# Kernel tuning notes

Hardware: AMD Instinct MI355X
Metric: run time of the kernel (lower is better)

Reference implementation:

```python
import jax, jax.numpy as jnp
import numpy as np

GROUP_SIZE = 64
M, K, N, RANK = 4096, 4096, 4096, 32


def setup_inputs() -> dict:
    key = jax.random.key(0)
    ks = jax.random.split(key, 7)
    x = jax.random.normal(ks[0], (M, K), dtype=jnp.float32)
    # int4 weight residual in [-8, 7]
    q_w = jax.random.randint(ks[1], (K, N), -8, 8, dtype=jnp.int32)
    # positive per-group weight scales, shape (K // group_size, N)
    wscales = jax.random.uniform(ks[2], (K // GROUP_SIZE, N), dtype=jnp.float32) * 0.01 + 1e-4
    lora_down = jax.random.normal(ks[3], (K, RANK), dtype=jnp.float32) * 0.02
    lora_up = jax.random.normal(ks[4], (RANK, N), dtype=jnp.float32) * 0.02
    # smoothing factors, strictly positive
    smooth = jax.random.uniform(ks[5], (K,), dtype=jnp.float32) + 0.5
    bias = jax.random.normal(ks[6], (N,), dtype=jnp.float32)
    return {"x": x, "q_w": q_w, "wscales": wscales, "lora_down": lora_down,
            "lora_up": lora_up, "smooth": smooth, "bias": bias}


def reference(x, q_w, wscales, lora_down, lora_up, smooth, bias):
    G = GROUP_SIZE
    m, k = x.shape
    n = q_w.shape[1]
    ng = k // G  # groups along K

    # smooth activation: move outliers into weights
    x_smooth = x / smooth[None, :]

    # per-group symmetric int4 quantize + dequantize of activations
    xg = x_smooth.reshape(m, ng, G)
    ascales = jnp.maximum(jnp.max(jnp.abs(xg), axis=-1) / 7.0, 1e-8)  # (m, ng)
    qx = jnp.clip(jnp.round(xg / ascales[..., None]), -8.0, 7.0)
    x_dq = (qx * ascales[..., None]).reshape(m, k)

    # dequantize int4 weight residual: grouped along K
    W_dq = (q_w.astype(jnp.float32).reshape(ng, G, n) * wscales[:, None, :]).reshape(k, n)

    # simulated int4 GEMM + fp LoRA residual + bias
    y_main = x_dq @ W_dq
    y_lora = (x @ lora_down) @ lora_up
    return y_main + y_lora + bias[None, :]
```

## Files before the change

### kernel.cpp

```cpp
#include <hip/hip_runtime.h>
#include <hip/hip_bf16.h>
#include <stdint.h>

#define GSIZE 64
#define MDIM 4096
#define KDIM 4096
#define NDIM 4096
#define RANK 32
#define KE   4160
#define NG   64
#define NSPLIT 8

typedef __bf16 bf16x4 __attribute__((ext_vector_type(4)));
typedef __bf16 bf16x8 __attribute__((ext_vector_type(8)));
typedef float  f32x4  __attribute__((ext_vector_type(4)));

#define GPTR(p) ((__attribute__((address_space(1))) void*)(uintptr_t)(p))
#define LPTR(p) ((__attribute__((address_space(3))) void*)(p))


__global__ __launch_bounds__(256) void k_lorat(const float* __restrict__ x,
                                               const float* __restrict__ ld,
                                               float* __restrict__ tws) {
    __shared__ __attribute__((aligned(16))) char smem[10240];
    __bf16* AsL = (__bf16*)smem;
    __bf16* BsL = (__bf16*)(smem + 8192);
    int b   = blockIdx.x;
    int tid = threadIdx.x;
    int m0    = (b & 31) * 128;
    int sp    = b >> 5;
    int kbase = sp * 512;
    int lane = tid & 63;
    int wave = tid >> 6;
    int quad = lane >> 4;
    int mrow = lane & 15;

    f32x4 z = {0.f, 0.f, 0.f, 0.f};
    f32x4 acc[2][2];
    acc[0][0] = z; acc[0][1] = z; acc[1][0] = z; acc[1][1] = z;

    for (int step = 0; step < 16; ++step) {
        int kk = kbase + step * 32;
        #pragma unroll
        for (int it = 0; it < 2; ++it) {
            int slot = it * 256 + tid;
            int r = slot >> 2;
            int g = (slot & 3) ^ (r & 3);
            const float* src = x + (size_t)(m0 + r) * KDIM + kk + g * 8;
            float4 a0 = *(const float4*)src;
            float4 a1 = *(const float4*)(src + 4);
            bf16x8 v = {(__bf16)a0.x, (__bf16)a0.y, (__bf16)a0.z, (__bf16)a0.w,
                        (__bf16)a1.x, (__bf16)a1.y, (__bf16)a1.z, (__bf16)a1.w};
            *(bf16x8*)(AsL + slot * 8) = v;
        }
        #pragma unroll
        for (int i2 = 0; i2 < 4; ++i2) {
            int j = i2 * 256 + tid;
            int r = j >> 5, n = j & 31;
            BsL[n * 32 + r] = (__bf16)ld[(size_t)(kk + r) * RANK + n];
        }
        __syncthreads();
        bf16x8 av[2], bv[2];
        #pragma unroll
        for (int i = 0; i < 2; ++i) {
            int row  = wave * 32 + i * 16 + mrow;
            int slot = row * 4 + (quad ^ (row & 3));
            av[i] = *(const bf16x8*)(AsL + slot * 8);
        }
        #pragma unroll
        for (int j = 0; j < 2; ++j)
            bv[j] = *(const bf16x8*)(BsL + (j * 16 + mrow) * 32 + quad * 8);
        #pragma unroll
        for (int i = 0; i < 2; ++i)
            #pragma unroll
            for (int j = 0; j < 2; ++j)
                acc[i][j] = __builtin_amdgcn_mfma_f32_16x16x32_bf16(av[i], bv[j], acc[i][j], 0, 0, 0);
        __syncthreads();
    }
    float* tout = tws + (size_t)sp * MDIM * RANK;
    #pragma unroll
    for (int i = 0; i < 2; ++i)
        #pragma unroll
        for (int j = 0; j < 2; ++j)
            #pragma unroll
            for (int r = 0; r < 4; ++r) {
                int rowg = m0 + wave * 32 + i * 16 + quad * 4 + r;
                int col  = j * 16 + mrow;
                tout[(size_t)rowg * RANK + col] = acc[i][j][r];
            }
}

__global__ __launch_bounds__(256) void k_wprep(const int*   __restrict__ qw,
                                               const float* __restrict__ wsc,
                                               const float* __restrict__ lu,
                                               __bf16* __restrict__ Wt) {
    __shared__ __attribute__((aligned(16))) __bf16 tile[64][68];
    int widx = blockIdx.x;
    int tid  = threadIdx.x;
    int n0 = (widx & 63) * 64;
    int kt = widx >> 6;
    int k0 = kt * 64;
    int tr = tid >> 4;
    int tc = (tid & 15) * 4;
    if (kt < NG) {
        float4 ws = *(const float4*)(wsc + (size_t)kt * NDIM + n0 + tc);
        #pragma unroll
        for (int r = tr; r < 64; r += 16) {
            int4 q = *(const int4*)(qw + (size_t)(k0 + r) * NDIM + n0 + tc);
            tile[r][tc + 0] = (__bf16)((float)q.x * ws.x);
            tile[r][tc + 1] = (__bf16)((float)q.y * ws.y);
            tile[r][tc + 2] = (__bf16)((float)q.z * ws.z);
            tile[r][tc + 3] = (__bf16)((float)q.w * ws.w);
        }
    } else {
        #pragma unroll
        for (int r = tr; r < 64; r += 16) {
            if (r < RANK) {
                float4 lv = *(const float4*)(lu + (size_t)r * NDIM + n0 + tc);
                tile[r][tc + 0] = (__bf16)lv.x;
                tile[r][tc + 1] = (__bf16)lv.y;
                tile[r][tc + 2] = (__bf16)lv.z;
                tile[r][tc + 3] = (__bf16)lv.w;
            } else {
                tile[r][tc + 0] = (__bf16)0.f;
                tile[r][tc + 1] = (__bf16)0.f;
                tile[r][tc + 2] = (__bf16)0.f;
                tile[r][tc + 3] = (__bf16)0.f;
            }
        }
    }
    __syncthreads();
    int nn = tid >> 3;
    int ks = (tid & 7) * 8;
    #pragma unroll
    for (int p = 0; p < 2; ++p) {
        int n = nn + p * 32;
        bf16x8 v;
        #pragma unroll
        for (int e = 0; e < 8; ++e) v[e] = tile[ks + e][n];
        *(bf16x8*)(Wt + (size_t)(n0 + n) * KE + k0 + ks) = v;
    }
}

__global__ __launch_bounds__(256) void k_quant(const float* __restrict__ x,
                                               const float* __restrict__ smooth,
                                               __bf16* __restrict__ A) {
    int row = blockIdx.x;
    int tid = threadIdx.x;
    const float4* xr4 = (const float4*)(x + (size_t)row * KDIM);
    const float4* sm4 = (const float4*)smooth;
    __bf16* ar = A + (size_t)row * KE;
    #pragma unroll
    for (int p = 0; p < 4; ++p) {
        int i4 = p * 256 + tid;
        float4 xv = xr4[i4];
        float4 sv = sm4[i4];
        float4 xs = {xv.x * __builtin_amdgcn_rcpf(sv.x),
                     xv.y * __builtin_amdgcn_rcpf(sv.y),
                     xv.z * __builtin_amdgcn_rcpf(sv.z),
                     xv.w * __builtin_amdgcn_rcpf(sv.w)};
        float a = fmaxf(fmaxf(fabsf(xs.x), fabsf(xs.y)),
                        fmaxf(fabsf(xs.z), fabsf(xs.w)));
        #pragma unroll
        for (int off = 1; off < 16; off <<= 1)
            a = fmaxf(a, __shfl_xor(a, off, 64));
        float ascale = fmaxf(a * (1.0f / 7.0f), 1e-8f);
        float rin = __builtin_amdgcn_rcpf(ascale);
        float q0 = fminf(fmaxf(rintf(xs.x * rin), -8.f), 7.f);
        float q1 = fminf(fmaxf(rintf(xs.y * rin), -8.f), 7.f);
        float q2 = fminf(fmaxf(rintf(xs.z * rin), -8.f), 7.f);
        float q3 = fminf(fmaxf(rintf(xs.w * rin), -8.f), 7.f);
        bf16x4 av = {(__bf16)(q0 * ascale), (__bf16)(q1 * ascale),
                     (__bf16)(q2 * ascale), (__bf16)(q3 * ascale)};
        *(bf16x4*)(ar + i4 * 4) = av;
    }
}

__global__ __launch_bounds__(256) void k_fin(const float* __restrict__ tws,
                                             __bf16* __restrict__ A) {
    int idx = blockIdx.x * 256 + threadIdx.x;
    int m = idx >> 4, cq = idx & 15;
    int c = cq * 4;
    bf16x4 v = {(__bf16)0.f, (__bf16)0.f, (__bf16)0.f, (__bf16)0.f};
    if (c < RANK) {
        f32x4 s = {0.f, 0.f, 0.f, 0.f};
        #pragma unroll
        for (int sp = 0; sp < NSPLIT; ++sp) {
            f32x4 p = *(const f32x4*)(tws + ((size_t)sp * MDIM + m) * RANK + c);
            s.x += p.x; s.y += p.y; s.z += p.z; s.w += p.w;
        }
        v[0] = (__bf16)s.x; v[1] = (__bf16)s.y; v[2] = (__bf16)s.z; v[3] = (__bf16)s.w;
    }
    *(bf16x4*)(A + (size_t)m * KE + KDIM + c) = v;
}

#define NT (KE / 64)
#define HS 8192
#define BS 16384

#define STAGE(ldsbase, gb, kt, half) do {                                     \
    int _k0 = (kt) * 64;                                                      \
    _Pragma("unroll")                                                         \
    for (int _it = 0; _it < 2; ++_it) {                                       \
        int _c = _it * 512 + tid;                                             \
        int _r = _c >> 3;                                                     \
        int _g = (_c & 7) ^ (_r & 7);                                         \
        __builtin_amdgcn_global_load_lds(                                     \
            GPTR((gb) + (size_t)((half) * 128 + _r) * KE + _k0 + _g * 8),     \
            LPTR((char*)(ldsbase) + (_it * 512 + wave * 64) * 16),            \
            16, 0, 0);                                                        \
    } } while (0)

#define RD_A(dst, base, qm) do {                                              \
    _Pragma("unroll")                                                         \
    for (int _i = 0; _i < 4; ++_i) {                                          \
        int _row = (qm) * 128 + wm * 64 + _i * 16 + mrow;                     \
        dst[0][_i] = *(const bf16x8*)((const char*)(base) + _row * 128 + ga0 * 16); \
        dst[1][_i] = *(const bf16x8*)((const char*)(base) + _row * 128 + ga1 * 16); \
    } } while (0)

#define RD_B(dst, base, qn) do {                                              \
    _Pragma("unroll")                                                         \
    for (int _j = 0; _j < 2; ++_j) {                                          \
        int _row = (qn) * 128 + wn * 32 + _j * 16 + mrow;                     \
        dst[0][_j] = *(const bf16x8*)((const char*)(base) + _row * 128 + ga0 * 16); \
        dst[1][_j] = *(const bf16x8*)((const char*)(base) + _row * 128 + ga1 * 16); \
    } } while (0)

#define MMA(qm, qn, AV, BV) do {                                              \
    _Pragma("unroll")                                                         \
    for (int _i = 0; _i < 4; ++_i)                                            \
        _Pragma("unroll")                                                     \
        for (int _j = 0; _j < 2; ++_j) {                                      \
            acc[qm][qn][_i][_j] = __builtin_amdgcn_mfma_f32_16x16x32_bf16(    \
                AV[0][_i], BV[0][_j], acc[qm][qn][_i][_j], 0, 0, 0);          \
            acc[qm][qn][_i][_j] = __builtin_amdgcn_mfma_f32_16x16x32_bf16(    \
                AV[1][_i], BV[1][_j], acc[qm][qn][_i][_j], 0, 0, 0);          \
        } } while (0)

#define SBAR0() __builtin_amdgcn_sched_barrier(0)

__global__ __launch_bounds__(512, 2) void k_gemm(const __bf16* __restrict__ A,
                                                 const __bf16* __restrict__ Wt,
                                                 const float*  __restrict__ bias,
                                                 float* __restrict__ out) {
    __shared__ __attribute__((aligned(16))) __bf16 As[2 * BS];
    __shared__ __attribute__((aligned(16))) __bf16 Bs[2 * BS];
    int tid  = threadIdx.x;
    int lane = tid & 63;
    int wave = tid >> 6;
    int quad = lane >> 4;
    int mrow = lane & 15;
    int wm = wave >> 2;
    int wn = wave & 3;

    int lin = blockIdx.y * 16 + blockIdx.x;
    int swz = (lin & 7) * 32 + (lin >> 3);
    int m0 = (swz >> 4) * 256, n0 = (swz & 15) * 256;

    const __bf16* Ab = A  + (size_t)m0 * KE;
    const __bf16* Bb = Wt + (size_t)n0 * KE;

    int ga0 = quad ^ (mrow & 7);
    int ga1 = (quad + 4) ^ (mrow & 7);

    f32x4 z = {0.f, 0.f, 0.f, 0.f};
    f32x4 acc[2][2][4][2];
    #pragma unroll
    for (int a = 0; a < 2; ++a)
        #pragma unroll
        for (int b = 0; b < 2; ++b)
            #pragma unroll
            for (int i = 0; i < 4; ++i)
                #pragma unroll
                for (int j = 0; j < 2; ++j) acc[a][b][i][j] = z;

    STAGE(As,           Ab, 0, 0);
    STAGE(Bs + HS,      Bb, 0, 1);
    STAGE(Bs,           Bb, 0, 0);
    STAGE(As + HS,      Ab, 0, 1);
    STAGE(As + BS,      Ab, 1, 0);
    STAGE(Bs + BS + HS, Bb, 1, 1);
    asm volatile("s_waitcnt vmcnt(4)" ::: "memory");
    __builtin_amdgcn_s_barrier();
    SBAR0();

    bf16x8 av0[2][4], av1[2][4], bv0[2][2], bv1[2][2];
    RD_A(av0, As, 0);
    RD_B(bv0, Bs, 0);
    SBAR0();

    for (int t = 0; t < NT; ++t) {
        int cur = t & 1;
        const __bf16* Acur = As + cur * BS;
        const __bf16* Bcur = Bs + cur * BS;
        __bf16* Anx = As + (cur ^ 1) * BS;
        __bf16* Bnx = Bs + (cur ^ 1) * BS;
        __bf16* Acu = As + cur * BS;
        __bf16* Bcu = Bs + cur * BS;
        bool s1 = (t + 1 < NT), s2 = (t + 2 < NT);

        if (s1) STAGE(Bnx, Bb, t + 1, 0);
        RD_B(bv1, Bcur, 1);
        SBAR0();
        asm volatile("s_waitcnt lgkmcnt(4)" ::: "memory");
        SBAR0();
        __builtin_amdgcn_s_setprio(1);
        MMA(0, 0, av0, bv0);
        __builtin_amdgcn_s_setprio(0);

        if (s1) STAGE(Anx + HS, Ab, t + 1, 1);
        RD_A(av1, Acur, 1);
        SBAR0();
        asm volatile("s_waitcnt lgkmcnt(8)" ::: "memory");
        SBAR0();
        __builtin_amdgcn_s_setprio(1);
        MMA(0, 1, av0, bv1);
        __builtin_amdgcn_s_setprio(0);
        __builtin_amdgcn_s_barrier();
        SBAR0();

        if (s2) STAGE(Acu, Ab, t + 2, 0);
        SBAR0();
        asm volatile("s_waitcnt lgkmcnt(0)" ::: "memory");
        SBAR0();
        __builtin_amdgcn_s_setprio(1);
        MMA(1, 1, av1, bv1);
        __builtin_amdgcn_s_setprio(0);
        if (s2) { asm volatile("s_waitcnt vmcnt(2)" ::: "memory"); }
        else    { asm volatile("s_waitcnt vmcnt(0)" ::: "memory"); }
        __builtin_amdgcn_s_barrier();
        SBAR0();

        if (s2) STAGE(Bcu + HS, Bb, t + 2, 1);
        if (s1) RD_A(av0, Anx, 0);
        SBAR0();
        __builtin_amdgcn_s_setprio(1);
        MMA(1, 0, av1, bv0);
        __builtin_amdgcn_s_setprio(0);
        if (s1) RD_B(bv0, Bnx, 0);
        SBAR0();
    }

    #pragma unroll
    for (int qn = 0; qn < 2; ++qn)
        #pragma unroll
        for (int j = 0; j < 2; ++j) {
            int col = n0 + qn * 128 + wn * 32 + j * 16 + mrow;
            float bvs = bias[col];
            #pragma unroll
            for (int qm = 0; qm < 2; ++qm)
                #pragma unroll
                for (int i = 0; i < 4; ++i) {
                    int rbase = m0 + qm * 128 + wm * 64 + i * 16 + quad * 4;
                    #pragma unroll
                    for (int r = 0; r < 4; ++r)
                        __builtin_nontemporal_store(acc[qm][qn][i][j][r] + bvs,
                                                    &out[(size_t)(rbase + r) * NDIM + col]);
                }
        }
}

extern "C" void kernel_launch(void* const* d_in, const int* in_sizes, int n_in,
                              void* d_out, int out_size, void* d_ws, size_t ws_size,
                              hipStream_t stream) {
    const float* x    = (const float*)d_in[0];
    const int*   qw   = (const int*)  d_in[1];
    const float* wsc  = (const float*)d_in[2];
    const float* ld   = (const float*)d_in[3];
    const float* lu   = (const float*)d_in[4];
    const float* sm   = (const float*)d_in[5];
    const float* bias = (const float*)d_in[6];
    float* out = (float*)d_out;

    char* ws = (char*)d_ws;
    __bf16* A   = (__bf16*)ws;
    __bf16* Wt  = (__bf16*)(ws + (size_t)MDIM * KE * 2);
    float*  tws = (float*) (ws + (size_t)MDIM * KE * 4);

    k_lorat<<<32 * NSPLIT, 256, 0, stream>>>(x, ld, tws);
    k_wprep<<<65 * 64, 256, 0, stream>>>(qw, wsc, lu, Wt);
    k_quant<<<MDIM, 256, 0, stream>>>(x, sm, A);
    k_fin<<<(MDIM * 16) / 256, 256, 0, stream>>>(tws, A);
    k_gemm<<<dim3(NDIM / 256, MDIM / 256), 512, 0, stream>>>(A, Wt, bias, out);
}
```

Measured before the change: 326.5 us.

## Fuse LoRA-down, weight prep and activation quant into one prep kernel

Merges three preprocessing kernels (LoRA down-projection partials, weight dequant/transposition, activation smoothing+quantization) into a single 512-thread launch with block-index dispatch. The LoRA blocks also quantize the x tile they already cover, so x is read by the same block for both uses, and two launches are removed. The trade-off is heterogeneous blocks sharing one launch config and fewer waves of smaller per-thread work in the weight-prep path.

After: 306.5 us. 1.07x faster.

```diff
diff --git a/kernel.cpp b/kernel.cpp
--- a/kernel.cpp
+++ b/kernel.cpp
@@ -11,6 +11,10 @@
 #define NG   64
 #define NSPLIT 8
 
+#define N_LORATQ 256
+#define N_WPREP  (65 * 64)
+#define NBLOCKS  (N_LORATQ + N_WPREP)
+
 typedef __bf16 bf16x4 __attribute__((ext_vector_type(4)));
 typedef __bf16 bf16x8 __attribute__((ext_vector_type(8)));
 typedef float  f32x4  __attribute__((ext_vector_type(4)));
@@ -18,161 +22,151 @@
 #define GPTR(p) ((__attribute__((address_space(1))) void*)(uintptr_t)(p))
 #define LPTR(p) ((__attribute__((address_space(3))) void*)(p))
 
-
-__global__ __launch_bounds__(256) void k_lorat(const float* __restrict__ x,
-                                               const float* __restrict__ ld,
-                                               float* __restrict__ tws) {
+__global__ __launch_bounds__(512) void k_prep(const float* __restrict__ x,
+                                              const int*   __restrict__ qw,
+                                              const float* __restrict__ wsc,
+                                              const float* __restrict__ ld,
+                                              const float* __restrict__ lu,
+                                              const float* __restrict__ smooth,
+                                              __bf16* __restrict__ A,
+                                              __bf16* __restrict__ Wt,
+                                              float* __restrict__ tws) {
     __shared__ __attribute__((aligned(16))) char smem[10240];
-    __bf16* AsL = (__bf16*)smem;
-    __bf16* BsL = (__bf16*)(smem + 8192);
     int b   = blockIdx.x;
     int tid = threadIdx.x;
-    int m0    = (b & 31) * 128;
-    int sp    = b >> 5;
-    int kbase = sp * 512;
-    int lane = tid & 63;
-    int wave = tid >> 6;
-    int quad = lane >> 4;
-    int mrow = lane & 15;
-
-    f32x4 z = {0.f, 0.f, 0.f, 0.f};
-    f32x4 acc[2][2];
-    acc[0][0] = z; acc[0][1] = z; acc[1][0] = z; acc[1][1] = z;
-
-    for (int step = 0; step < 16; ++step) {
-        int kk = kbase + step * 32;
-        #pragma unroll
-        for (int it = 0; it < 2; ++it) {
-            int slot = it * 256 + tid;
-            int r = slot >> 2;
-            int g = (slot & 3) ^ (r & 3);
-            const float* src = x + (size_t)(m0 + r) * KDIM + kk + g * 8;
-            float4 a0 = *(const float4*)src;
-            float4 a1 = *(const float4*)(src + 4);
-            bf16x8 v = {(__bf16)a0.x, (__bf16)a0.y, (__bf16)a0.z, (__bf16)a0.w,
-                        (__bf16)a1.x, (__bf16)a1.y, (__bf16)a1.z, (__bf16)a1.w};
-            *(bf16x8*)(AsL + slot * 8) = v;
-        }
-        #pragma unroll
-        for (int i2 = 0; i2 < 4; ++i2) {
-            int j = i2 * 256 + tid;
-            int r = j >> 5, n = j & 31;
-            BsL[n * 32 + r] = (__bf16)ld[(size_t)(kk + r) * RANK + n];
+
+    if (b < N_LORATQ) {
+        int m0    = (b & 31) * 128;
+        int sp    = b >> 5;
+        int kbase = sp * 512;
+
+        {
+            int c4 = tid & 127;
+            int r0 = tid >> 7;
+            float4 sv = *(const float4*)(smooth + kbase + c4 * 4);
+            float4 si = {__builtin_amdgcn_rcpf(sv.x), __builtin_amdgcn_rcpf(sv.y),
+                         __builtin_amdgcn_rcpf(sv.z), __builtin_amdgcn_rcpf(sv.w)};
+            #pragma unroll 4
+            for (int p = 0; p < 32; ++p) {
+                int row = r0 + p * 4;
+                float4 xv = *(const float4*)(x + (size_t)(m0 + row) * KDIM + kbase + c4 * 4);
+                float4 xs = {xv.x * si.x, xv.y * si.y, xv.z * si.z, xv.w * si.w};
+                float a = fmaxf(fmaxf(fabsf(xs.x), fabsf(xs.y)),
+                                fmaxf(fabsf(xs.z), fabsf(xs.w)));
+                #pragma unroll
+                for (int off = 1; off < 16; off <<= 1)
+                    a = fmaxf(a, __shfl_xor(a, off, 64));
+                float ascale = fmaxf(a * (1.0f / 7.0f), 1e-8f);
+                float rin = __builtin_amdgcn_rcpf(ascale);
+                float q0 = fminf(fmaxf(rintf(xs.x * rin), -8.f), 7.f);
+                float q1 = fminf(fmaxf(rintf(xs.y * rin), -8.f), 7.f);
+                float q2 = fminf(fmaxf(rintf(xs.z * rin), -8.f), 7.f);
+                float q3 = fminf(fmaxf(rintf(xs.w * rin), -8.f), 7.f);
+                bf16x4 av = {(__bf16)(q0 * ascale), (__bf16)(q1 * ascale),
+                             (__bf16)(q2 * ascale), (__bf16)(q3 * ascale)};
+                *(bf16x4*)(A + (size_t)(m0 + row) * KE + kbase + c4 * 4) = av;
+            }
+        }
+
+        __bf16* AsL = (__bf16*)smem;
+        __bf16* BsL = (__bf16*)(smem + 8192);
+        int lane = tid & 63;
+        int wave = tid >> 6;
+        int quad = lane >> 4;
+        int mrow = lane & 15;
+
+        f32x4 z = {0.f, 0.f, 0.f, 0.f};
+        f32x4 acc[2];
+        acc[0] = z; acc[1] = z;
+
+        for (int step = 0; step < 16; ++step) {
+            int kk = kbase + step * 32;
+            {
+                int slot = tid;
+                int r = slot >> 2;
+                int g = (slot & 3) ^ (r & 3);
+                const float* src = x + (size_t)(m0 + r) * KDIM + kk + g * 8;
+                float4 a0 = *(const float4*)src;
+                float4 a1 = *(const float4*)(src + 4);
+                bf16x8 v = {(__bf16)a0.x, (__bf16)a0.y, (__bf16)a0.z, (__bf16)a0.w,
+                            (__bf16)a1.x, (__bf16)a1.y, (__bf16)a1.z, (__bf16)a1.w};
+                *(bf16x8*)(AsL + slot * 8) = v;
+            }
+            #pragma unroll
+            for (int i2 = 0; i2 < 2; ++i2) {
+                int j = i2 * 512 + tid;
+                int r = j >> 5, n = j & 31;
+                BsL[n * 32 + r] = (__bf16)ld[(size_t)(kk + r) * RANK + n];
+            }
+            __syncthreads();
+            bf16x8 av, bv[2];
+            {
+                int row  = wave * 16 + mrow;
+                int slot = row * 4 + (quad ^ (row & 3));
+                av = *(const bf16x8*)(AsL + slot * 8);
+            }
+            #pragma unroll
+            for (int j = 0; j < 2; ++j)
+                bv[j] = *(const bf16x8*)(BsL + (j * 16 + mrow) * 32 + quad * 8);
+            #pragma unroll
+            for (int j = 0; j < 2; ++j)
+                acc[j] = __builtin_amdgcn_mfma_f32_16x16x32_bf16(av, bv[j], acc[j], 0, 0, 0);
+            __syncthreads();
+        }
+        float* tout = tws + (size_t)sp * MDIM * RANK;
+        #pragma unroll
+        for (int j = 0; j < 2; ++j)
+            #pragma unroll
+            for (int r = 0; r < 4; ++r) {
+                int rowg = m0 + wave * 16 + quad * 4 + r;
+                int col  = j * 16 + mrow;
+                tout[(size_t)rowg * RANK + col] = acc[j][r];
+            }
+        return;
+    }
+
+    {
+        __bf16 (*tile)[68] = (__bf16(*)[68])smem;
+        int widx = b - N_LORATQ;
+        int n0 = (widx & 63) * 64;
+        int kt = widx >> 6;
+        int k0 = kt * 64;
+        int tr = tid >> 4;
+        int tc = (tid & 15) * 4;
+        if (kt < NG) {
+            float4 ws = *(const float4*)(wsc + (size_t)kt * NDIM + n0 + tc);
+            #pragma unroll
+            for (int r = tr; r < 64; r += 32) {
+                int4 q = *(const int4*)(qw + (size_t)(k0 + r) * NDIM + n0 + tc);
+                tile[r][tc + 0] = (__bf16)((float)q.x * ws.x);
+                tile[r][tc + 1] = (__bf16)((float)q.y * ws.y);
+                tile[r][tc + 2] = (__bf16)((float)q.z * ws.z);
+                tile[r][tc + 3] = (__bf16)((float)q.w * ws.w);
+            }
+        } else {
+            #pragma unroll
+            for (int r = tr; r < 64; r += 32) {
+                if (r < RANK) {
+                    float4 lv = *(const float4*)(lu + (size_t)r * NDIM + n0 + tc);
+                    tile[r][tc + 0] = (__bf16)lv.x;
+                    tile[r][tc + 1] = (__bf16)lv.y;
+                    tile[r][tc + 2] = (__bf16)lv.z;
+                    tile[r][tc + 3] = (__bf16)lv.w;
+                } else {
+                    tile[r][tc + 0] = (__bf16)0.f;
+                    tile[r][tc + 1] = (__bf16)0.f;
+                    tile[r][tc + 2] = (__bf16)0.f;
+                    tile[r][tc + 3] = (__bf16)0.f;
+                }
+            }
         }
         __syncthreads();
-        bf16x8 av[2], bv[2];
-        #pragma unroll
-        for (int i = 0; i < 2; ++i) {
-            int row  = wave * 32 + i * 16 + mrow;
-            int slot = row * 4 + (quad ^ (row & 3));
-            av[i] = *(const bf16x8*)(AsL + slot * 8);
-        }
-        #pragma unroll
-        for (int j = 0; j < 2; ++j)
-            bv[j] = *(const bf16x8*)(BsL + (j * 16 + mrow) * 32 + quad * 8);
-        #pragma unroll
-        for (int i = 0; i < 2; ++i)
-            #pragma unroll
-            for (int j = 0; j < 2; ++j)
-                acc[i][j] = __builtin_amdgcn_mfma_f32_16x16x32_bf16(av[i], bv[j], acc[i][j], 0, 0, 0);
-        __syncthreads();
-    }
-    float* tout = tws + (size_t)sp * MDIM * RANK;
-    #pragma unroll
-    for (int i = 0; i < 2; ++i)
-        #pragma unroll
-        for (int j = 0; j < 2; ++j)
-            #pragma unroll
-            for (int r = 0; r < 4; ++r) {
-                int rowg = m0 + wave * 32 + i * 16 + quad * 4 + r;
-                int col  = j * 16 + mrow;
-                tout[(size_t)rowg * RANK + col] = acc[i][j][r];
-            }
-}
-
-__global__ __launch_bounds__(256) void k_wprep(const int*   __restrict__ qw,
-                                               const float* __restrict__ wsc,
-                                               const float* __restrict__ lu,
-                                               __bf16* __restrict__ Wt) {
-    __shared__ __attribute__((aligned(16))) __bf16 tile[64][68];
-    int widx = blockIdx.x;
-    int tid  = threadIdx.x;
-    int n0 = (widx & 63) * 64;
-    int kt = widx >> 6;
-    int k0 = kt * 64;
-    int tr = tid >> 4;
-    int tc = (tid & 15) * 4;
-    if (kt < NG) {
-        float4 ws = *(const float4*)(wsc + (size_t)kt * NDIM + n0 + tc);
-        #pragma unroll
-        for (int r = tr; r < 64; r += 16) {
-            int4 q = *(const int4*)(qw + (size_t)(k0 + r) * NDIM + n0 + tc);
-            tile[r][tc + 0] = (__bf16)((float)q.x * ws.x);
-            tile[r][tc + 1] = (__bf16)((float)q.y * ws.y);
-            tile[r][tc + 2] = (__bf16)((float)q.z * ws.z);
-            tile[r][tc + 3] = (__bf16)((float)q.w * ws.w);
-        }
-    } else {
-        #pragma unroll
-        for (int r = tr; r < 64; r += 16) {
-            if (r < RANK) {
-                float4 lv = *(const float4*)(lu + (size_t)r * NDIM + n0 + tc);
-                tile[r][tc + 0] = (__bf16)lv.x;
-                tile[r][tc + 1] = (__bf16)lv.y;
-                tile[r][tc + 2] = (__bf16)lv.z;
-                tile[r][tc + 3] = (__bf16)lv.w;
-            } else {
-                tile[r][tc + 0] = (__bf16)0.f;
-                tile[r][tc + 1] = (__bf16)0.f;
-                tile[r][tc + 2] = (__bf16)0.f;
-                tile[r][tc + 3] = (__bf16)0.f;
-            }
-        }
-    }
-    __syncthreads();
-    int nn = tid >> 3;
-    int ks = (tid & 7) * 8;
-    #pragma unroll
-    for (int p = 0; p < 2; ++p) {
-        int n = nn + p * 32;
+        int nn = tid >> 3;
+        int ks = (tid & 7) * 8;
         bf16x8 v;
         #pragma unroll
-        for (int e = 0; e < 8; ++e) v[e] = tile[ks + e][n];
-        *(bf16x8*)(Wt + (size_t)(n0 + n) * KE + k0 + ks) = v;
-    }
-}
-
-__global__ __launch_bounds__(256) void k_quant(const float* __restrict__ x,
-                                               const float* __restrict__ smooth,
-                                               __bf16* __restrict__ A) {
-    int row = blockIdx.x;
-    int tid = threadIdx.x;
-    const float4* xr4 = (const float4*)(x + (size_t)row * KDIM);
-    const float4* sm4 = (const float4*)smooth;
-    __bf16* ar = A + (size_t)row * KE;
-    #pragma unroll
-    for (int p = 0; p < 4; ++p) {
-        int i4 = p * 256 + tid;
-        float4 xv = xr4[i4];
-        float4 sv = sm4[i4];
-        float4 xs = {xv.x * __builtin_amdgcn_rcpf(sv.x),
-                     xv.y * __builtin_amdgcn_rcpf(sv.y),
-                     xv.z * __builtin_amdgcn_rcpf(sv.z),
-                     xv.w * __builtin_amdgcn_rcpf(sv.w)};
-        float a = fmaxf(fmaxf(fabsf(xs.x), fabsf(xs.y)),
-                        fmaxf(fabsf(xs.z), fabsf(xs.w)));
-        #pragma unroll
-        for (int off = 1; off < 16; off <<= 1)
-            a = fmaxf(a, __shfl_xor(a, off, 64));
-        float ascale = fmaxf(a * (1.0f / 7.0f), 1e-8f);
-        float rin = __builtin_amdgcn_rcpf(ascale);
-        float q0 = fminf(fmaxf(rintf(xs.x * rin), -8.f), 7.f);
-        float q1 = fminf(fmaxf(rintf(xs.y * rin), -8.f), 7.f);
-        float q2 = fminf(fmaxf(rintf(xs.z * rin), -8.f), 7.f);
-        float q3 = fminf(fmaxf(rintf(xs.w * rin), -8.f), 7.f);
-        bf16x4 av = {(__bf16)(q0 * ascale), (__bf16)(q1 * ascale),
-                     (__bf16)(q2 * ascale), (__bf16)(q3 * ascale)};
-        *(bf16x4*)(ar + i4 * 4) = av;
+        for (int e = 0; e < 8; ++e) v[e] = tile[ks + e][nn];
+        *(bf16x8*)(Wt + (size_t)(n0 + nn) * KE + k0 + ks) = v;
     }
 }
 
@@ -378,9 +372,7 @@
     __bf16* Wt  = (__bf16*)(ws + (size_t)MDIM * KE * 2);
     float*  tws = (float*) (ws + (size_t)MDIM * KE * 4);
 
-    k_lorat<<<32 * NSPLIT, 256, 0, stream>>>(x, ld, tws);
-    k_wprep<<<65 * 64, 256, 0, stream>>>(qw, wsc, lu, Wt);
-    k_quant<<<MDIM, 256, 0, stream>>>(x, sm, A);
+    k_prep<<<NBLOCKS, 512, 0, stream>>>(x, qw, wsc, ld, lu, sm, A, Wt, tws);
     k_fin<<<(MDIM * 16) / 256, 256, 0, stream>>>(tws, A);
     k_gemm<<<dim3(NDIM / 256, MDIM / 256), 512, 0, stream>>>(A, Wt, bias, out);
 }
```
